# Optimization experiments

Measured on AMD Instinct MI355X. Metric: run time of the kernel, lower is better.

The kernel has to match this reference:

```python
import jax, jax.numpy as jnp
import numpy as np
from jax import lax

V = 33      # n_vertices
EPS = 1e-5  # instance-norm eps


def _resize_bilinear(x, oh, ow):
    # torch F.interpolate bilinear, align_corners=False, antialias=False
    b, c, H, W = x.shape
    def coords(out, size):
        src = (jnp.arange(out, dtype=jnp.float32) + 0.5) * (size / out) - 0.5
        i0 = jnp.clip(jnp.floor(src).astype(jnp.int32), 0, size - 1)
        i1 = jnp.clip(i0 + 1, 0, size - 1)
        f = jnp.clip(src - i0.astype(jnp.float32), 0.0, 1.0)
        return i0, i1, f
    y0, y1, fy = coords(oh, H)
    x0, x1, fx = coords(ow, W)
    rows = x[:, :, y0, :] * (1 - fy)[None, None, :, None] + x[:, :, y1, :] * fy[None, None, :, None]
    return rows[:, :, :, x0] * (1 - fx) + rows[:, :, :, x1] * fx


def _conv_s2(x, w, b):
    y = lax.conv_general_dilated(x, w, (2, 2), [(1, 1), (1, 1)],
                                 dimension_numbers=('NCHW', 'OIHW', 'NCHW'))
    return y + b[None, :, None, None]


def _lrelu(x):
    return jnp.where(x >= 0, x, 0.2 * x)


def _inorm(x, g, be):
    m = x.mean((2, 3), keepdims=True)
    v = x.var((2, 3), keepdims=True)
    return (x - m) / jnp.sqrt(v + EPS) * g[None, :, None, None] + be[None, :, None, None]


def _ailut_transform(imgs, luts, vertices):
    # imgs (b,3,H,W); luts (b,3,V,V,V) indexed [out_c, ib, ig, ir]; vertices (b,3,V)
    b, c, H, W = imgs.shape
    N = H * W
    x = jnp.clip(imgs, 0.0, 1.0).reshape(b, 3, N)
    ss = jax.vmap(jax.vmap(lambda v, q: jnp.searchsorted(v, q, side='right')))
    idx = jnp.clip(ss(vertices, x) - 1, 0, V - 2)            # (b,3,N)
    v0 = jnp.take_along_axis(vertices, idx, axis=-1)
    v1 = jnp.take_along_axis(vertices, idx + 1, axis=-1)
    frac = jnp.clip((x - v0) / jnp.maximum(v1 - v0, 1e-10), 0.0, 1.0)
    ir, ig, ibl = idx[:, 0], idx[:, 1], idx[:, 2]            # (b,N) each
    fr, fg, fb = frac[:, 0], frac[:, 1], frac[:, 2]
    lut_flat = luts.reshape(b, 3, V * V * V)
    out = jnp.zeros((b, 3, N), imgs.dtype)
    for db in (0, 1):
        wb = fb if db else 1.0 - fb
        for dg in (0, 1):
            wg = fg if dg else 1.0 - fg
            for dr in (0, 1):
                w = wb * wg * (fr if dr else 1.0 - fr)       # (b,N)
                flat = ((ibl + db) * V + (ig + dg)) * V + (ir + dr)
                vals = jnp.take_along_axis(lut_flat, jnp.broadcast_to(flat[:, None, :], (b, 3, N)), axis=-1)
                out = out + w[:, None, :] * vals
    return out.reshape(b, 3, H, W)


def setup_inputs() -> dict:
    key = jax.random.key(0)
    ks = jax.random.split(key, 32)
    n = lambda k, s: jax.random.normal(k, s, jnp.float32) * 0.05
    inp = {'imgs': jax.random.uniform(ks[0], (2, 3, 2048, 2048), jnp.float32)}
    chans = [(3, 16), (16, 32), (32, 64), (64, 128), (128, 128)]
    for i, (ci, co) in enumerate(chans, start=1):
        inp[f'w{i}'] = n(ks[2 * i], (co, ci, 3, 3))
        inp[f'b{i}'] = n(ks[2 * i + 1], (co,))
        if i <= 4:
            inp[f'g{i}'] = jnp.ones((co,), jnp.float32)
            inp[f'be{i}'] = jnp.zeros((co,), jnp.float32)
    inp['wgen_w'] = n(ks[12], (512, 3))
    inp['wgen_b'] = n(ks[13], (3,))
    inp['basis_w'] = n(ks[14], (3, 3 * V ** 3))
    inp['ada_w'] = n(ks[15], (512, 3 * (V - 1)))
    inp['ada_b'] = n(ks[16], (3 * (V - 1),))
    return inp


def reference(imgs, w1, b1, g1, be1, w2, b2, g2, be2, w3, b3, g3, be3,
              w4, b4, g4, be4, w5, b5, wgen_w, wgen_b, basis_w, ada_w, ada_b):
    b = imgs.shape[0]
    x = _resize_bilinear(imgs, 256, 256)
    for (w, bb, g, be) in ((w1, b1, g1, be1), (w2, b2, g2, be2),
                           (w3, b3, g3, be3), (w4, b4, g4, be4)):
        x = _inorm(_lrelu(_conv_s2(x, w, bb)), g, be)
    x = _lrelu(_conv_s2(x, w5, b5))                      # (b,128,8,8); dropout is identity at eval
    x = x.reshape(b, 128, 2, 4, 2, 4).mean((3, 5)).reshape(b, 512)  # AdaptiveAvgPool2d(2)
    weights = x @ wgen_w + wgen_b                        # (b,3) rank weights
    luts = (weights @ basis_w).reshape(b, 3, V, V, V)
    intervals = jax.nn.softmax((x @ ada_w + ada_b).reshape(b, 3, V - 1), axis=-1)
    vertices = jnp.pad(jnp.cumsum(intervals, -1), ((0, 0), (0, 0), (1, 0)))  # (b,3,V)
    return _ailut_transform(imgs, luts, vertices)
```

## Files before the change

### kernel.cpp

```cpp
#include <hip/hip_runtime.h>
#include <hip/hip_fp16.h>
#include <cstdint>
#include <cstddef>

#define VCUBE 35937
#define LUT_CH 107811

__global__ __launch_bounds__(256) void conv1_fused(const float* __restrict__ imgs,
    const float* __restrict__ w, const float* __restrict__ bias,
    float* __restrict__ out) {
  __shared__ float s_in[3*3*34];
  __shared__ float s_w[16*3*9];
  int bid = blockIdx.x;
  int owt = bid & 7; int oh = (bid >> 3) & 127; int b = bid >> 10;
  int t = threadIdx.x;
  int ow0 = owt * 16;
  int iwbase = 2*ow0 - 1;
  int ihbase = 2*oh - 1;
  for (int i = t; i < 3*3*34; i += 256) {
    int x = i % 34; int rest = i / 34; int kh = rest % 3; int ci = rest / 3;
    int ih = ihbase + kh;
    int iw = iwbase + x;
    float v = 0.f;
    if (ih >= 0 && ih < 256 && iw >= 0 && iw < 256) {
      const float* p = imgs + (size_t)(b*3+ci) * 2048 * 2048;
      int y0 = ih*8 + 3, x0 = iw*8 + 3;
      const float* r0 = p + (size_t)y0*2048 + x0;
      const float* r1 = r0 + 2048;
      float a = r0[0], bb = r0[1], c = r1[0], d = r1[1];
      float top = a + 0.5f*(bb - a);
      float bot = c + 0.5f*(d - c);
      v = top + 0.5f*(bot - top);
    }
    s_in[i] = v;
  }
  for (int i = t; i < 16*3*9; i += 256) s_w[i] = w[i];
  __syncthreads();
  int owl = t & 15; int co = t >> 4;
  float acc = bias[co];
  const float* wp = s_w + co*27;
#pragma unroll
  for (int ci = 0; ci < 3; ci++) {
#pragma unroll
    for (int kh = 0; kh < 3; kh++) {
      const float* rp = s_in + (ci*3 + kh)*34 + 2*owl;
      acc = fmaf(rp[0], wp[ci*9 + kh*3 + 0], acc);
      acc = fmaf(rp[1], wp[ci*9 + kh*3 + 1], acc);
      acc = fmaf(rp[2], wp[ci*9 + kh*3 + 2], acc);
    }
  }
  acc = acc >= 0.f ? acc : 0.2f*acc;
  out[(((size_t)b*16 + co)*128 + oh)*128 + ow0 + owl] = acc;
}

template<int CI, int CO, int IS, int COPB, bool WLDS>
__global__ __launch_bounds__(256) void conv_row(const float* __restrict__ in,
    const float* __restrict__ w, const float* __restrict__ bias,
    float* __restrict__ out) {
  constexpr int OS = IS/2;
  constexpr int PW = IS + 2;
  constexpr int NG = CO/COPB;
  constexpr int E  = CI*3*PW;
  static_assert(COPB*OS == 256, "block mismatch");
  __shared__ float s_in[E];
  __shared__ float s_w[WLDS ? COPB*CI*9 : 1];
  int bid = blockIdx.x;
  int grp = bid % NG; int rest = bid / NG; int oh = rest % OS; int b = rest / OS;
  int t = threadIdx.x;
  int ihb = 2*oh - 1;
  for (int i = t; i < E; i += 256) {
    int x = i % PW; int r2 = i / PW; int kh = r2 % 3; int ci = r2 / 3;
    int ih = ihb + kh; int iw = x - 1;
    float v = 0.f;
    if (ih >= 0 && ih < IS && iw >= 0 && iw < IS)
      v = in[((size_t)(b*CI + ci)*IS + ih)*IS + iw];
    s_in[i] = v;
  }
  if (WLDS) {
    const float* wg = w + (size_t)grp*COPB*CI*9;
    for (int i = t; i < COPB*CI*9; i += 256) s_w[i] = wg[i];
  }
  __syncthreads();
  int ow = t % OS; int col = t / OS;
  int co = grp*COPB + col;
  float acc = bias[co];
  const float* wp = WLDS ? (s_w + col*CI*9) : (w + (size_t)co*CI*9);
  for (int ci = 0; ci < CI; ci++) {
    const float* rowp = s_in + ci*3*PW;
    const float* wc = wp + ci*9;
#pragma unroll
    for (int kh = 0; kh < 3; kh++) {
      const float* rp = rowp + kh*PW + 2*ow;
      acc = fmaf(rp[0], wc[kh*3 + 0], acc);
      acc = fmaf(rp[1], wc[kh*3 + 1], acc);
      acc = fmaf(rp[2], wc[kh*3 + 2], acc);
    }
  }
  acc = acc >= 0.f ? acc : 0.2f*acc;
  out[(((size_t)b*CO + co)*OS + oh)*OS + ow] = acc;
}

__global__ __launch_bounds__(256) void inorm_kernel(float* __restrict__ x,
    const float* __restrict__ g, const float* __restrict__ be, int C, int HW) {
  int plane = blockIdx.x;
  int c = plane % C;
  float* p = x + (size_t)plane * HW;
  int t = threadIdx.x;
  float s = 0.f, s2 = 0.f;
  for (int i = t; i < HW; i += 256) {
    float v = p[i];
    s += v;
    s2 = fmaf(v, v, s2);
  }
  __shared__ float ss[256], sq[256];
  ss[t] = s; sq[t] = s2;
  __syncthreads();
  for (int off = 128; off > 0; off >>= 1) {
    if (t < off) { ss[t] += ss[t + off]; sq[t] += sq[t + off]; }
    __syncthreads();
  }
  __shared__ float sc, sh;
  if (t == 0) {
    float inv_n = 1.0f / (float)HW;
    float mean = ss[0] * inv_n;
    float var  = sq[0] * inv_n - mean*mean;
    float scale = g[c] / sqrtf(var + 1e-5f);
    sc = scale;
    sh = be[c] - mean*scale;
  }
  __syncthreads();
  for (int i = t; i < HW; i += 256) p[i] = fmaf(p[i], sc, sh);
}

__global__ __launch_bounds__(128) void head_kernel(const float* __restrict__ x5,
    const float* __restrict__ wgen_w, const float* __restrict__ wgen_b,
    const float* __restrict__ ada_w, const float* __restrict__ ada_b,
    float* __restrict__ gweights, float* __restrict__ vertices,
    float* __restrict__ invtab, uint8_t* __restrict__ hints) {
  int b = blockIdx.x; int t = threadIdx.x;
  __shared__ float xv[512];
  __shared__ float logits[96];
  __shared__ float svp[99];
  for (int o = t; o < 512; o += 128) {
    int c = o >> 2; int h2 = (o >> 1) & 1; int w2 = o & 1;
    const float* p = x5 + ((size_t)(b*128 + c))*64 + h2*32 + w2*4;
    float s = 0.f;
#pragma unroll
    for (int h = 0; h < 4; h++)
#pragma unroll
      for (int ww = 0; ww < 4; ww++) s += p[h*8 + ww];
    xv[o] = s * (1.f/16.f);
  }
  __syncthreads();
  if (t < 96) {
    float s = ada_b[t];
    for (int k = 0; k < 512; k++) s = fmaf(xv[k], ada_w[k*96 + t], s);
    logits[t] = s;
  } else if (t < 99) {
    int j = t - 96;
    float s = wgen_b[j];
    for (int k = 0; k < 512; k++) s = fmaf(xv[k], wgen_w[k*3 + j], s);
    gweights[b*3 + j] = s;
  }
  __syncthreads();
  if (t < 3) {
    const float* l = logits + t*32;
    float m = l[0];
#pragma unroll
    for (int i = 1; i < 32; i++) m = fmaxf(m, l[i]);
    float e[32]; float sum = 0.f;
#pragma unroll
    for (int i = 0; i < 32; i++) { e[i] = expf(l[i] - m); sum += e[i]; }
    float inv = 1.0f / sum;
    float* vp = vertices + b*99 + t*33;
    svp[t*33] = 0.f; vp[0] = 0.f;
    float cum = 0.f;
#pragma unroll
    for (int i = 0; i < 32; i++) { cum = fmaf(e[i], inv, cum); svp[t*33 + i + 1] = cum; vp[i + 1] = cum; }
  }
  __syncthreads();
  if (t < 96) {
    int c = t >> 5, i = t & 31;
    float d = svp[c*33 + i + 1] - svp[c*33 + i];
    invtab[b*96 + t] = 1.0f / fmaxf(d, 1e-10f);
  }
  for (int e = t; e < 3072; e += 128) {
    int c = e >> 10; int bin = e & 1023;
    float q0 = (float)bin * (1.f/1024.f);
    const float* v = svp + c*33;
    int lo = 0, hi = 33;
    while (lo < hi) { int mid = (lo + hi) >> 1; if (v[mid] <= q0) lo = mid + 1; else hi = mid; }
    int idx = lo - 1; if (idx > 31) idx = 31;
    hints[b*3072 + e] = (uint8_t)idx;
  }
}

__global__ __launch_bounds__(256) void ecell_build(const float* __restrict__ basis_w,
    const float* __restrict__ gw, __half* __restrict__ ecell, int B) {
  int tid = blockIdx.x*256 + threadIdx.x;
  int total = B * 32768 * 3;
  if (tid >= total) return;
  int cc = tid % 3;
  int cell = tid / 3;
  int r = cell & 31; int g = (cell >> 5) & 31; int bl = (cell >> 10) & 31; int b = cell >> 15;
  float w0 = gw[b*3 + 0], w1 = gw[b*3 + 1], w2 = gw[b*3 + 2];
  union { __half h[8]; uint4 u; } pk;
#pragma unroll
  for (int dbl = 0; dbl < 2; dbl++)
#pragma unroll
    for (int dg = 0; dg < 2; dg++)
#pragma unroll
      for (int dr = 0; dr < 2; dr++) {
        int flat = cc*VCUBE + ((bl + dbl)*33 + (g + dg))*33 + (r + dr);
        float val = w0*basis_w[flat] + w1*basis_w[LUT_CH + flat] + w2*basis_w[2*LUT_CH + flat];
        pk.h[dbl*4 + dg*2 + dr] = __float2half(val);
      }
  *(uint4*)((uint16_t*)ecell + (size_t)cell*32 + cc*8) = pk.u;
}

__device__ __forceinline__ void lut_px(float R, float G, float Bl,
    const __half* __restrict__ ec, const float* sv, const float* sinv,
    const uint8_t* shint, float* o0, float* o1, float* o2) {
  float q[3] = { fminf(fmaxf(R, 0.f), 1.f), fminf(fmaxf(G, 0.f), 1.f), fminf(fmaxf(Bl, 0.f), 1.f) };
  int id[3]; float fr[3];
#pragma unroll
  for (int c = 0; c < 3; c++) {
    float qc = q[c];
    int bin = (int)(qc * 1024.f); bin = bin > 1023 ? 1023 : bin;
    int idx = shint[(c << 10) + bin];
    const float* v = sv + c*33;
#pragma unroll
    for (int it = 0; it < 3; it++)
      idx += (idx < 31 && v[idx + 1] <= qc) ? 1 : 0;
    float f = (qc - v[idx]) * sinv[(c << 5) + idx];
    fr[c] = fminf(fmaxf(f, 0.f), 1.f);
    id[c] = idx;
  }
  const __half* cell = ec + ((size_t)(((id[2] << 5) + id[1]) << 5) + id[0]) * 32;
  float fR = fr[0], fG = fr[1], fB = fr[2];
  float res[3];
#pragma unroll
  for (int cc = 0; cc < 3; cc++) {
    uint4 u = *(const uint4*)(cell + cc*8);
    const __half* h = (const __half*)&u;
    float f0 = __half2float(h[0]), f1 = __half2float(h[1]);
    float f2 = __half2float(h[2]), f3 = __half2float(h[3]);
    float f4 = __half2float(h[4]), f5 = __half2float(h[5]);
    float f6 = __half2float(h[6]), f7 = __half2float(h[7]);
    float l00 = fmaf(fR, f1 - f0, f0);
    float l01 = fmaf(fR, f3 - f2, f2);
    float L0  = fmaf(fG, l01 - l00, l00);
    float l10 = fmaf(fR, f5 - f4, f4);
    float l11 = fmaf(fR, f7 - f6, f6);
    float L1  = fmaf(fG, l11 - l10, l10);
    res[cc] = fmaf(fB, L1 - L0, L0);
  }
  *o0 = res[0]; *o1 = res[1]; *o2 = res[2];
}

__global__ __launch_bounds__(256) void transform_kernel(const float* __restrict__ imgs,
    const __half* __restrict__ ecell, const float* __restrict__ vert,
    const float* __restrict__ invtab, const unsigned int* __restrict__ hintw,
    float* __restrict__ out, int B) {
  const size_t N = 2048u*2048u;
  __shared__ float sv[99];
  __shared__ float sinv[96];
  __shared__ unsigned int shint_w[768];
  int b = blockIdx.x % B;
  int pblk = blockIdx.x / B;
  int t = threadIdx.x;
  if (t < 99) sv[t] = vert[b*99 + t];
  if (t < 96) sinv[t] = invtab[b*96 + t];
  for (int i = t; i < 768; i += 256) shint_w[i] = hintw[b*768 + i];
  __syncthreads();
  const uint8_t* shint = (const uint8_t*)shint_w;
  size_t pix = ((size_t)pblk*256 + t) * 4;
  const float* ip = imgs + (size_t)b*3*N;
  float* op = out + (size_t)b*3*N;
  const __half* ec = ecell + (size_t)b*1048576;
  float4 r  = *(const float4*)(ip + pix);
  float4 g  = *(const float4*)(ip + N + pix);
  float4 bb = *(const float4*)(ip + 2*N + pix);
  float4 o0, o1, o2;
  lut_px(r.x, g.x, bb.x, ec, sv, sinv, shint, &o0.x, &o1.x, &o2.x);
  lut_px(r.y, g.y, bb.y, ec, sv, sinv, shint, &o0.y, &o1.y, &o2.y);
  lut_px(r.z, g.z, bb.z, ec, sv, sinv, shint, &o0.z, &o1.z, &o2.z);
  lut_px(r.w, g.w, bb.w, ec, sv, sinv, shint, &o0.w, &o1.w, &o2.w);
  *(float4*)(op + pix) = o0;
  *(float4*)(op + N + pix) = o1;
  *(float4*)(op + 2*N + pix) = o2;
}

extern "C" void kernel_launch(void* const* d_in, const int* in_sizes, int n_in,
                              void* d_out, int out_size, void* d_ws, size_t ws_size,
                              hipStream_t stream) {
  const float* imgs = (const float*)d_in[0];
  const float* w1 = (const float*)d_in[1];  const float* b1 = (const float*)d_in[2];
  const float* g1 = (const float*)d_in[3];  const float* be1 = (const float*)d_in[4];
  const float* w2 = (const float*)d_in[5];  const float* b2 = (const float*)d_in[6];
  const float* g2 = (const float*)d_in[7];  const float* be2 = (const float*)d_in[8];
  const float* w3 = (const float*)d_in[9];  const float* b3 = (const float*)d_in[10];
  const float* g3 = (const float*)d_in[11]; const float* be3 = (const float*)d_in[12];
  const float* w4 = (const float*)d_in[13]; const float* b4 = (const float*)d_in[14];
  const float* g4 = (const float*)d_in[15]; const float* be4 = (const float*)d_in[16];
  const float* w5 = (const float*)d_in[17]; const float* b5 = (const float*)d_in[18];
  const float* wgen_w  = (const float*)d_in[19];
  const float* wgen_b  = (const float*)d_in[20];
  const float* basis_w = (const float*)d_in[21];
  const float* ada_w   = (const float*)d_in[22];
  const float* ada_b   = (const float*)d_in[23];
  float* out = (float*)d_out;

  const int B = in_sizes[0] / (3*2048*2048);

  char* wsb = (char*)d_ws;
  __half* ecell = (__half*)wsb;
  size_t A_bytes = (size_t)B * 2097152;
  float* x1 = (float*)wsb;
  float* x2 = x1 + (size_t)B*262144;
  float* x3 = x2 + (size_t)B*131072;
  float* x4 = x3 + (size_t)B*65536;
  float* x5 = x4 + (size_t)B*32768;
  float* tail = (float*)(wsb + A_bytes);
  float* gw   = tail;
  float* vert = gw + (size_t)B*4;
  float* invt = vert + (size_t)B*99;
  uint8_t* hints = (uint8_t*)(invt + (size_t)B*96);

  conv1_fused<<<B*1024, 256, 0, stream>>>(imgs, w1, b1, x1);
  inorm_kernel<<<B*16, 256, 0, stream>>>(x1, g1, be1, 16, 128*128);
  conv_row<16, 32, 128, 4, true><<<B*512, 256, 0, stream>>>(x1, w2, b2, x2);
  inorm_kernel<<<B*32, 256, 0, stream>>>(x2, g2, be2, 32, 64*64);
  conv_row<32, 64, 64, 8, true><<<B*256, 256, 0, stream>>>(x2, w3, b3, x3);
  inorm_kernel<<<B*64, 256, 0, stream>>>(x3, g3, be3, 64, 32*32);
  conv_row<64, 128, 32, 16, true><<<B*128, 256, 0, stream>>>(x3, w4, b4, x4);
  inorm_kernel<<<B*128, 256, 0, stream>>>(x4, g4, be4, 128, 16*16);
  conv_row<128, 128, 16, 32, false><<<B*32, 256, 0, stream>>>(x4, w5, b5, x5);
  head_kernel<<<B, 128, 0, stream>>>(x5, wgen_w, wgen_b, ada_w, ada_b, gw, vert, invt, hints);
  ecell_build<<<B*384, 256, 0, stream>>>(basis_w, gw, ecell, B);
  transform_kernel<<<B*4096, 256, 0, stream>>>(imgs, ecell, vert, invt,
                                               (const unsigned int*)hints, out, B);
}
```

Measured before the change: 488.6 us.

## Batch LUT gathers across four pixels and use nontemporal streaming I/O

The transform kernel now computes bin indices and fractions for all four pixels first, then issues all twelve 16-byte cell gathers together before the trilinear math, so more memory requests are in flight per thread. The sequential dependent vertex search is replaced by branchless comparisons over a padded shared vertex table, and the per-bin reciprocal table is replaced with a hardware rcp. Image loads and output stores use nontemporal hints to reduce cache pollution for the LUT, and launch bounds request higher occupancy. The risks are more register pressure from holding twelve uint4 values, and small numerical differences from the approximate reciprocal.

```diff
diff --git a/kernel.cpp b/kernel.cpp
--- a/kernel.cpp
+++ b/kernel.cpp
@@ -5,6 +5,8 @@
 
 #define VCUBE 35937
 #define LUT_CH 107811
+
+typedef float fx4 __attribute__((ext_vector_type(4)));
 
 __global__ __launch_bounds__(256) void conv1_fused(const float* __restrict__ imgs,
     const float* __restrict__ w, const float* __restrict__ bias,
@@ -218,59 +220,35 @@
   *(uint4*)((uint16_t*)ecell + (size_t)cell*32 + cc*8) = pk.u;
 }
 
-__device__ __forceinline__ void lut_px(float R, float G, float Bl,
-    const __half* __restrict__ ec, const float* sv, const float* sinv,
-    const uint8_t* shint, float* o0, float* o1, float* o2) {
-  float q[3] = { fminf(fmaxf(R, 0.f), 1.f), fminf(fmaxf(G, 0.f), 1.f), fminf(fmaxf(Bl, 0.f), 1.f) };
-  int id[3]; float fr[3];
-#pragma unroll
-  for (int c = 0; c < 3; c++) {
-    float qc = q[c];
-    int bin = (int)(qc * 1024.f); bin = bin > 1023 ? 1023 : bin;
-    int idx = shint[(c << 10) + bin];
-    const float* v = sv + c*33;
-#pragma unroll
-    for (int it = 0; it < 3; it++)
-      idx += (idx < 31 && v[idx + 1] <= qc) ? 1 : 0;
-    float f = (qc - v[idx]) * sinv[(c << 5) + idx];
-    fr[c] = fminf(fmaxf(f, 0.f), 1.f);
-    id[c] = idx;
-  }
-  const __half* cell = ec + ((size_t)(((id[2] << 5) + id[1]) << 5) + id[0]) * 32;
-  float fR = fr[0], fG = fr[1], fB = fr[2];
-  float res[3];
-#pragma unroll
-  for (int cc = 0; cc < 3; cc++) {
-    uint4 u = *(const uint4*)(cell + cc*8);
-    const __half* h = (const __half*)&u;
-    float f0 = __half2float(h[0]), f1 = __half2float(h[1]);
-    float f2 = __half2float(h[2]), f3 = __half2float(h[3]);
-    float f4 = __half2float(h[4]), f5 = __half2float(h[5]);
-    float f6 = __half2float(h[6]), f7 = __half2float(h[7]);
-    float l00 = fmaf(fR, f1 - f0, f0);
-    float l01 = fmaf(fR, f3 - f2, f2);
-    float L0  = fmaf(fG, l01 - l00, l00);
-    float l10 = fmaf(fR, f5 - f4, f4);
-    float l11 = fmaf(fR, f7 - f6, f6);
-    float L1  = fmaf(fG, l11 - l10, l10);
-    res[cc] = fmaf(fB, L1 - L0, L0);
-  }
-  *o0 = res[0]; *o1 = res[1]; *o2 = res[2];
-}
-
-__global__ __launch_bounds__(256) void transform_kernel(const float* __restrict__ imgs,
+__device__ __forceinline__ float trilerp_cell(uint4 u, float fR, float fG, float fB) {
+  const __half* h = (const __half*)&u;
+  float f0 = __half2float(h[0]), f1 = __half2float(h[1]);
+  float f2 = __half2float(h[2]), f3 = __half2float(h[3]);
+  float f4 = __half2float(h[4]), f5 = __half2float(h[5]);
+  float f6 = __half2float(h[6]), f7 = __half2float(h[7]);
+  float l00 = fmaf(fR, f1 - f0, f0);
+  float l01 = fmaf(fR, f3 - f2, f2);
+  float L0  = fmaf(fG, l01 - l00, l00);
+  float l10 = fmaf(fR, f5 - f4, f4);
+  float l11 = fmaf(fR, f7 - f6, f6);
+  float L1  = fmaf(fG, l11 - l10, l10);
+  return fmaf(fB, L1 - L0, L0);
+}
+
+__global__ __launch_bounds__(256, 4) void transform_kernel(const float* __restrict__ imgs,
     const __half* __restrict__ ecell, const float* __restrict__ vert,
     const float* __restrict__ invtab, const unsigned int* __restrict__ hintw,
     float* __restrict__ out, int B) {
   const size_t N = 2048u*2048u;
-  __shared__ float sv[99];
-  __shared__ float sinv[96];
+  __shared__ float sv[112];
   __shared__ unsigned int shint_w[768];
   int b = blockIdx.x % B;
   int pblk = blockIdx.x / B;
   int t = threadIdx.x;
-  if (t < 99) sv[t] = vert[b*99 + t];
-  if (t < 96) sinv[t] = invtab[b*96 + t];
+  if (t < 108) {
+    int c = t / 36, i = t - c*36;
+    sv[t] = (i < 33) ? vert[b*99 + c*33 + i] : 2.0f;
+  }
   for (int i = t; i < 768; i += 256) shint_w[i] = hintw[b*768 + i];
   __syncthreads();
   const uint8_t* shint = (const uint8_t*)shint_w;
@@ -278,17 +256,63 @@
   const float* ip = imgs + (size_t)b*3*N;
   float* op = out + (size_t)b*3*N;
   const __half* ec = ecell + (size_t)b*1048576;
-  float4 r  = *(const float4*)(ip + pix);
-  float4 g  = *(const float4*)(ip + N + pix);
-  float4 bb = *(const float4*)(ip + 2*N + pix);
-  float4 o0, o1, o2;
-  lut_px(r.x, g.x, bb.x, ec, sv, sinv, shint, &o0.x, &o1.x, &o2.x);
-  lut_px(r.y, g.y, bb.y, ec, sv, sinv, shint, &o0.y, &o1.y, &o2.y);
-  lut_px(r.z, g.z, bb.z, ec, sv, sinv, shint, &o0.z, &o1.z, &o2.z);
-  lut_px(r.w, g.w, bb.w, ec, sv, sinv, shint, &o0.w, &o1.w, &o2.w);
-  *(float4*)(op + pix) = o0;
-  *(float4*)(op + N + pix) = o1;
-  *(float4*)(op + 2*N + pix) = o2;
+
+  fx4 r  = __builtin_nontemporal_load((const fx4*)(ip + pix));
+  fx4 g  = __builtin_nontemporal_load((const fx4*)(ip + N + pix));
+  fx4 bb = __builtin_nontemporal_load((const fx4*)(ip + 2*N + pix));
+
+  float qv[3][4] = { { r.x, r.y, r.z, r.w },
+                     { g.x, g.y, g.z, g.w },
+                     { bb.x, bb.y, bb.z, bb.w } };
+  int   idxv[3][4];
+  float frv[3][4];
+
+#pragma unroll
+  for (int c = 0; c < 3; c++) {
+#pragma unroll
+    for (int p = 0; p < 4; p++) {
+      float qc = fminf(fmaxf(qv[c][p], 0.f), 1.f);
+      int bin = (int)(qc * 1024.f); bin = bin > 1023 ? 1023 : bin;
+      int h = shint[(c << 10) + bin];
+      const float* vv = sv + c*36 + h;
+      float v0 = vv[0], v1 = vv[1], v2 = vv[2], v3 = vv[3], v4 = vv[4];
+      int cnt = (int)(v1 <= qc) + (int)(v2 <= qc) + (int)(v3 <= qc);
+      int cmax = 31 - h; cnt = cnt < cmax ? cnt : cmax;
+      float lo = v0, hi = v1;
+      lo = cnt >= 1 ? v1 : lo;  hi = cnt >= 1 ? v2 : hi;
+      lo = cnt >= 2 ? v2 : lo;  hi = cnt >= 2 ? v3 : hi;
+      lo = cnt >= 3 ? v3 : lo;  hi = cnt >= 3 ? v4 : hi;
+      idxv[c][p] = h + cnt;
+      float f = (qc - lo) * __builtin_amdgcn_rcpf(fmaxf(hi - lo, 1e-10f));
+      frv[c][p] = fminf(fmaxf(f, 0.f), 1.f);
+    }
+  }
+
+  uint4 u0[4], u1[4], u2[4];
+#pragma unroll
+  for (int p = 0; p < 4; p++) {
+    const __half* cell = ec +
+        ((size_t)(((idxv[2][p] << 5) + idxv[1][p]) << 5) + idxv[0][p]) * 32;
+    u0[p] = *(const uint4*)(cell);
+    u1[p] = *(const uint4*)(cell + 8);
+    u2[p] = *(const uint4*)(cell + 16);
+  }
+
+  fx4 o0, o1, o2;
+#pragma unroll
+  for (int p = 0; p < 4; p++) {
+    float fR = frv[0][p], fG = frv[1][p], fB = frv[2][p];
+    float a0 = trilerp_cell(u0[p], fR, fG, fB);
+    float a1 = trilerp_cell(u1[p], fR, fG, fB);
+    float a2 = trilerp_cell(u2[p], fR, fG, fB);
+    if (p == 0) { o0.x = a0; o1.x = a1; o2.x = a2; }
+    if (p == 1) { o0.y = a0; o1.y = a1; o2.y = a2; }
+    if (p == 2) { o0.z = a0; o1.z = a1; o2.z = a2; }
+    if (p == 3) { o0.w = a0; o1.w = a1; o2.w = a2; }
+  }
+  __builtin_nontemporal_store(o0, (fx4*)(op + pix));
+  __builtin_nontemporal_store(o1, (fx4*)(op + N + pix));
+  __builtin_nontemporal_store(o2, (fx4*)(op + 2*N + pix));
 }
 
 extern "C" void kernel_launch(void* const* d_in, const int* in_sizes, int n_in,
```

New measurement: 453.9 us. 1.08x faster.
